# Optimization experiments

Measured on AMD Instinct MI355X. Metric: run time of the kernel, lower is better.

The kernel has to match this reference:

```python
import jax, jax.numpy as jnp
import numpy as np

B, N, E, L = 64, 50000, 1600000, 20
BN_EPS = 1e-5


def setup_inputs() -> dict:
    key = jax.random.key(0)
    ks = jax.random.split(key, 8)
    x = jax.random.normal(ks[0], (B, N), dtype=jnp.float32)
    edge_index = jax.random.randint(ks[1], (2, E), 0, N, dtype=jnp.int32)
    alpha = jax.random.normal(ks[2], (E,), dtype=jnp.float32)
    bias = jax.random.normal(ks[3], (E,), dtype=jnp.float32)
    # LazyLinear(num_labels) on [B, N] features
    W = jax.random.normal(ks[4], (L, N), dtype=jnp.float32) / np.sqrt(N)
    b_lin = jax.random.normal(ks[5], (L,), dtype=jnp.float32) * 0.01
    # LazyBatchNorm1d affine params over N features
    gamma = jnp.ones((N,), dtype=jnp.float32)
    beta = jnp.zeros((N,), dtype=jnp.float32)
    return {"x": x, "edge_index": edge_index, "alpha": alpha, "bias": bias,
            "W": W, "b_lin": b_lin, "gamma": gamma, "beta": beta}


def reference(x, edge_index, alpha, bias, W, b_lin, gamma, beta):
    src, dst = edge_index[0], edge_index[1]
    # gather per-edge source features and apply per-edge affine: [B, E]
    x_e = alpha * x[:, src] + bias
    # scatter-mean into destination nodes: [B, N]
    sums = jnp.zeros((x.shape[0], N), dtype=x.dtype).at[:, dst].add(x_e)
    counts = jnp.zeros((N,), dtype=x.dtype).at[dst].add(1.0)
    x_hat = sums / jnp.maximum(counts, 1.0)
    out = jnp.tanh(x_hat)
    # linear head: [B, L]
    pred = x_hat @ W.T + b_lin
    # BatchNorm1d (training mode: batch stats, biased variance)
    mu = jnp.mean(out, axis=0)
    var = jnp.var(out, axis=0)
    bn = (out - mu) / jnp.sqrt(var + BN_EPS) * gamma + beta
    return (pred, bn)
```

## Files before the change

kernel.cpp:

```cpp
#include <hip/hip_runtime.h>
#include <math.h>

#define NB 64
#define NL 20
#define BN_EPS 1e-5f

#define BIN_W 64
#define NBIN 782
#define NBINP 1024
#define BIN_CAP 2560
#define CHUNK 4096

__device__ __forceinline__ unsigned short f2bf(float f) {
    unsigned u = __float_as_uint(f);
    unsigned r = u + 0x7fff + ((u >> 16) & 1);
    return (unsigned short)(r >> 16);
}
__device__ __forceinline__ float bf2f(unsigned short h) {
    return __uint_as_float(((unsigned)h) << 16);
}

__global__ __launch_bounds__(256) void transpose_kernel(
    const float* __restrict__ x, unsigned short* __restrict__ xTb, int Nn) {
    __shared__ float tile[64][65];
    int n0 = blockIdx.x * 64;
    int ln = threadIdx.x & 63;
    int wv = threadIdx.x >> 6;
    for (int r = wv; r < 64; r += 4) {
        int col = n0 + ln;
        tile[r][ln] = (col < Nn) ? x[r * Nn + col] : 0.f;
    }
    __syncthreads();
    for (int r = wv; r < 64; r += 4) {
        int node = n0 + r;
        if (node < Nn) xTb[(size_t)node * 64 + ln] = f2bf(tile[ln][r]);
    }
}

__global__ __launch_bounds__(1024) void binsort_kernel(
    const int* __restrict__ src, const int* __restrict__ dst,
    const float* __restrict__ alpha, const float* __restrict__ bias,
    int* __restrict__ cursor, uint2* __restrict__ paybins, int E) {
    __shared__ unsigned hist[NBINP];
    __shared__ unsigned scn[NBINP];
    __shared__ unsigned gbase[NBINP];
    __shared__ unsigned wsum[16];
    __shared__ uint2 ord[CHUNK];

    int tid = threadIdx.x;
    int e0 = blockIdx.x * CHUNK;

    hist[tid] = 0;
    __syncthreads();

    uint2 pay[4];
    unsigned rk[4];
    int bn[4];
    #pragma unroll
    for (int k = 0; k < 4; ++k) {
        int e = e0 + k * 1024 + tid;
        bn[k] = -1;
        if (e < E) {
            int d = dst[e];
            int b = d >> 6;
            int dl = d & 63;
            pay[k].x = (unsigned)src[e] | ((unsigned)f2bf(alpha[e]) << 16);
            pay[k].y = (unsigned)f2bf(bias[e]) | ((unsigned)dl << 16) |
                       ((unsigned)b << 22);
            bn[k] = b;
            rk[k] = atomicAdd(&hist[b], 1u);
        }
    }
    __syncthreads();

    unsigned v = hist[tid];
    unsigned incl = v;
    #pragma unroll
    for (int off = 1; off < 64; off <<= 1) {
        unsigned t = __shfl_up(incl, off, 64);
        if ((tid & 63) >= off) incl += t;
    }
    if ((tid & 63) == 63) wsum[tid >> 6] = incl;
    __syncthreads();
    if (tid < 16) {
        unsigned y = wsum[tid];
        unsigned yi = y;
        #pragma unroll
        for (int off = 1; off < 16; off <<= 1) {
            unsigned t = __shfl_up(yi, off, 64);
            if (tid >= off) yi += t;
        }
        wsum[tid] = yi - y;
    }
    __syncthreads();
    unsigned excl = incl - v + wsum[tid >> 6];
    scn[tid] = excl;
    if (v > 0) gbase[tid] = atomicAdd(&cursor[tid], (int)v);
    __syncthreads();

    #pragma unroll
    for (int k = 0; k < 4; ++k)
        if (bn[k] >= 0) ord[scn[bn[k]] + rk[k]] = pay[k];
    __syncthreads();

    int cc = E - e0;
    if (cc > CHUNK) cc = CHUNK;
    for (int p = tid; p < cc; p += 1024) {
        uint2 w = ord[p];
        unsigned b = w.y >> 22;
        unsigned di = gbase[b] + ((unsigned)p - scn[b]);
        if (di < BIN_CAP)
            paybins[(size_t)b * BIN_CAP + di] = w;
    }
}

__global__ __launch_bounds__(512) void pull_fin2_kernel(
    const int* __restrict__ cursor, const uint2* __restrict__ paybins,
    const unsigned short* __restrict__ xTb, const float* __restrict__ W,
    const float* __restrict__ gamma, const float* __restrict__ beta,
    float* __restrict__ pred_part, float* __restrict__ bn, int Nn) {
    __shared__ __align__(16) char smem[33280];
    uint2* ed = (uint2*)smem;
    float (*xh)[65] = (float (*)[65])smem;
    float (*th)[65] = (float (*)[65])(smem + 16640);

    __shared__ float wl[NL][64];
    __shared__ unsigned h2[64], b2[64], c2[64];
    __shared__ float mu_s[64], a_s[64], be_s[64];

    int bin = blockIdx.x;
    int tid = threadIdx.x;
    int ln = tid & 63;
    int w = tid >> 6;
    int n0 = bin * 64;

    int cnt = cursor[bin];
    if (cnt > BIN_CAP) cnt = BIN_CAP;
    const uint2* pb = paybins + (size_t)bin * BIN_CAP;

    for (int i = tid; i < NL * 64; i += 512) {
        int l = i >> 6, j = i & 63;
        wl[l][j] = (n0 + j < Nn) ? W[l * Nn + n0 + j] : 0.f;
    }
    if (tid < 64) { h2[tid] = 0; c2[tid] = 0; }
    __syncthreads();

    uint2 myp[5];
    int nm = 0;
    for (int i = tid; i < cnt; i += 512) {
        uint2 p = pb[i];
        myp[nm++] = p;
        atomicAdd(&h2[(p.y >> 16) & 63], 1u);
    }
    __syncthreads();

    if (tid < 64) {
        unsigned v = h2[tid];
        unsigned incl = v;
        #pragma unroll
        for (int off = 1; off < 64; off <<= 1) {
            unsigned t = __shfl_up(incl, off, 64);
            if (tid >= off) incl += t;
        }
        b2[tid] = incl - v;
    }
    __syncthreads();

    for (int k = 0; k < nm; ++k) {
        unsigned dl = (myp[k].y >> 16) & 63;
        unsigned r = atomicAdd(&c2[dl], 1u);
        ed[b2[dl] + r] = myp[k];
    }
    __syncthreads();

    float xh_reg[8], th_reg[8];
    #pragma unroll
    for (int k = 0; k < 8; ++k) {
        int dl = w * 8 + k;
        int node = n0 + dl;
        int n = (int)h2[dl];
        unsigned bs = b2[dl];
        float a0 = 0.f, a1 = 0.f, a2 = 0.f, a3 = 0.f, bsum = 0.f;
        int j = 0;
        for (; j + 3 < n; j += 4) {
            uint2 e0 = ed[bs + j];
            uint2 e1 = ed[bs + j + 1];
            uint2 e2 = ed[bs + j + 2];
            uint2 e3 = ed[bs + j + 3];
            bsum += __uint_as_float((e0.y & 0xffffu) << 16) +
                    __uint_as_float((e1.y & 0xffffu) << 16) +
                    __uint_as_float((e2.y & 0xffffu) << 16) +
                    __uint_as_float((e3.y & 0xffffu) << 16);
            a0 = fmaf(__uint_as_float(e0.x & 0xffff0000u),
                      bf2f(xTb[(size_t)(e0.x & 0xffffu) * 64 + ln]), a0);
            a1 = fmaf(__uint_as_float(e1.x & 0xffff0000u),
                      bf2f(xTb[(size_t)(e1.x & 0xffffu) * 64 + ln]), a1);
            a2 = fmaf(__uint_as_float(e2.x & 0xffff0000u),
                      bf2f(xTb[(size_t)(e2.x & 0xffffu) * 64 + ln]), a2);
            a3 = fmaf(__uint_as_float(e3.x & 0xffff0000u),
                      bf2f(xTb[(size_t)(e3.x & 0xffffu) * 64 + ln]), a3);
        }
        for (; j < n; ++j) {
            uint2 e0 = ed[bs + j];
            bsum += __uint_as_float((e0.y & 0xffffu) << 16);
            a0 = fmaf(__uint_as_float(e0.x & 0xffff0000u),
                      bf2f(xTb[(size_t)(e0.x & 0xffffu) * 64 + ln]), a0);
        }
        float xhat = 0.f;
        if (node < Nn)
            xhat = ((a0 + a1) + (a2 + a3) + bsum) / fmaxf((float)n, 1.0f);
        xh_reg[k] = xhat;
        float tv = tanhf(xhat);
        th_reg[k] = tv;

        float s = tv, q = tv * tv;
        #pragma unroll
        for (int off = 32; off > 0; off >>= 1) {
            s += __shfl_xor(s, off, 64);
            q += __shfl_xor(q, off, 64);
        }
        if (ln == 0) {
            float mu = s * (1.0f / 64.0f);
            float var = fmaxf(q * (1.0f / 64.0f) - mu * mu, 0.f);
            float inv = rsqrtf(var + BN_EPS);
            float gm = 1.f, bt = 0.f;
            if (node < Nn) { gm = gamma[node]; bt = beta[node]; }
            mu_s[dl] = mu;
            a_s[dl] = inv * gm;
            be_s[dl] = bt;
        }
    }
    __syncthreads();

    #pragma unroll
    for (int k = 0; k < 8; ++k) {
        xh[w * 8 + k][ln] = xh_reg[k];
        th[w * 8 + k][ln] = th_reg[k];
    }
    __syncthreads();

    {
        float acc[3] = {0.f, 0.f, 0.f};
        for (int n = 0; n < 64; ++n) {
            float xv = xh[n][ln];
            #pragma unroll
            for (int k = 0; k < 3; ++k) {
                int l = w + k * 8;
                if (l < NL) acc[k] = fmaf(xv, wl[l][n], acc[k]);
            }
        }
        #pragma unroll
        for (int k = 0; k < 3; ++k) {
            int l = w + k * 8;
            if (l < NL)
                pred_part[(size_t)bin * (NB * NL) + ln * NL + l] = acc[k];
        }
    }

    for (int idx = tid; idx < 64 * 64; idx += 512) {
        int noff = idx & 63, bb = idx >> 6;
        int node = n0 + noff;
        if (node < Nn)
            bn[bb * Nn + node] =
                fmaf(th[noff][bb] - mu_s[noff], a_s[noff], be_s[noff]);
    }
}

__global__ __launch_bounds__(256) void reduce_pred_kernel(
    const float* __restrict__ part, const float* __restrict__ b_lin,
    float* __restrict__ pred, int nblk) {
    int out = blockIdx.x * 4 + (threadIdx.x >> 6);
    if (out >= NB * NL) return;
    int ln = threadIdx.x & 63;
    float s = 0.f;
    for (int i = ln; i < nblk; i += 64)
        s += part[(size_t)i * (NB * NL) + out];
    #pragma unroll
    for (int off = 32; off > 0; off >>= 1)
        s += __shfl_xor(s, off, 64);
    if (ln == 0) pred[out] = b_lin[out % NL] + s;
}

extern "C" void kernel_launch(void* const* d_in, const int* in_sizes, int n_in,
                              void* d_out, int out_size, void* d_ws, size_t ws_size,
                              hipStream_t stream) {
    const float* x     = (const float*)d_in[0];
    const int*   ei    = (const int*)d_in[1];
    const float* alpha = (const float*)d_in[2];
    const float* bias  = (const float*)d_in[3];
    const float* W     = (const float*)d_in[4];
    const float* b_lin = (const float*)d_in[5];
    const float* gamma = (const float*)d_in[6];
    const float* beta  = (const float*)d_in[7];

    const int Nn = in_sizes[0] / NB;
    const int E  = in_sizes[1] / 2;
    const int* src = ei;
    const int* dst = ei + E;

    const int ntile = (Nn + 63) / 64;

    uint2*          paybins = (uint2*)d_ws;
    unsigned short* xTb     = (unsigned short*)(paybins + (size_t)NBIN * BIN_CAP);
    int*            cursor  = (int*)(xTb + (size_t)Nn * 64);
    float*          pred_part = (float*)(cursor + NBIN);

    float* pred = (float*)d_out;
    float* bn   = pred + NB * NL;

    hipMemsetAsync(cursor, 0, NBIN * sizeof(int), stream);

    transpose_kernel<<<ntile, 256, 0, stream>>>(x, xTb, Nn);
    binsort_kernel<<<(E + CHUNK - 1) / CHUNK, 1024, 0, stream>>>(
        src, dst, alpha, bias, cursor, paybins, E);
    pull_fin2_kernel<<<NBIN, 512, 0, stream>>>(cursor, paybins, xTb, W,
                                               gamma, beta, pred_part, bn, Nn);
    reduce_pred_kernel<<<(NB * NL + 3) / 4, 256, 0, stream>>>(
        pred_part, b_lin, pred, NBIN);
}
```

Measured before the change: 212.3 us.

## Halve destination bin width and scatter binned edges directly to global memory

Destination bins shrink from 64 to 32 nodes, which doubles the bin count and halves per-bin capacity. The pull kernel now runs 256-thread blocks over 32 nodes each, with the payload loads unrolled into five fixed registers. The binsort kernel drops the shared-memory local reorder and writes each edge payload straight to its global bin slot, which removes a scan and two barriers but makes the global writes less coalesced. The partial-pred buffer doubles in size, so the final reduction reads twice as much, and the smaller bin capacity raises the risk of dropped edges if a bin overflows.

```diff
diff --git a/kernel.cpp b/kernel.cpp
--- a/kernel.cpp
+++ b/kernel.cpp
@@ -5,10 +5,10 @@
 #define NL 20
 #define BN_EPS 1e-5f
 
-#define BIN_W 64
-#define NBIN 782
-#define NBINP 1024
-#define BIN_CAP 2560
+#define BIN_W 32
+#define NBIN 1563
+#define NBINP 2048
+#define BIN_CAP 1280
 #define CHUNK 4096
 
 __device__ __forceinline__ unsigned short f2bf(float f) {
@@ -42,15 +42,13 @@
     const float* __restrict__ alpha, const float* __restrict__ bias,
     int* __restrict__ cursor, uint2* __restrict__ paybins, int E) {
     __shared__ unsigned hist[NBINP];
-    __shared__ unsigned scn[NBINP];
     __shared__ unsigned gbase[NBINP];
-    __shared__ unsigned wsum[16];
-    __shared__ uint2 ord[CHUNK];
 
     int tid = threadIdx.x;
     int e0 = blockIdx.x * CHUNK;
 
     hist[tid] = 0;
+    hist[tid + 1024] = 0;
     __syncthreads();
 
     uint2 pay[4];
@@ -62,103 +60,85 @@
         bn[k] = -1;
         if (e < E) {
             int d = dst[e];
-            int b = d >> 6;
-            int dl = d & 63;
+            int b = d >> 5;
+            int dl = d & 31;
             pay[k].x = (unsigned)src[e] | ((unsigned)f2bf(alpha[e]) << 16);
             pay[k].y = (unsigned)f2bf(bias[e]) | ((unsigned)dl << 16) |
-                       ((unsigned)b << 22);
+                       ((unsigned)b << 21);
             bn[k] = b;
             rk[k] = atomicAdd(&hist[b], 1u);
         }
     }
     __syncthreads();
 
-    unsigned v = hist[tid];
-    unsigned incl = v;
-    #pragma unroll
-    for (int off = 1; off < 64; off <<= 1) {
-        unsigned t = __shfl_up(incl, off, 64);
-        if ((tid & 63) >= off) incl += t;
-    }
-    if ((tid & 63) == 63) wsum[tid >> 6] = incl;
-    __syncthreads();
-    if (tid < 16) {
-        unsigned y = wsum[tid];
-        unsigned yi = y;
-        #pragma unroll
-        for (int off = 1; off < 16; off <<= 1) {
-            unsigned t = __shfl_up(yi, off, 64);
-            if (tid >= off) yi += t;
-        }
-        wsum[tid] = yi - y;
-    }
-    __syncthreads();
-    unsigned excl = incl - v + wsum[tid >> 6];
-    scn[tid] = excl;
-    if (v > 0) gbase[tid] = atomicAdd(&cursor[tid], (int)v);
-    __syncthreads();
-
-    #pragma unroll
-    for (int k = 0; k < 4; ++k)
-        if (bn[k] >= 0) ord[scn[bn[k]] + rk[k]] = pay[k];
-    __syncthreads();
-
-    int cc = E - e0;
-    if (cc > CHUNK) cc = CHUNK;
-    for (int p = tid; p < cc; p += 1024) {
-        uint2 w = ord[p];
-        unsigned b = w.y >> 22;
-        unsigned di = gbase[b] + ((unsigned)p - scn[b]);
-        if (di < BIN_CAP)
-            paybins[(size_t)b * BIN_CAP + di] = w;
-    }
-}
-
-__global__ __launch_bounds__(512) void pull_fin2_kernel(
+    for (int i = tid; i < NBINP; i += 1024) {
+        unsigned v = hist[i];
+        if (v > 0) gbase[i] = (unsigned)atomicAdd(&cursor[i], (int)v);
+    }
+    __syncthreads();
+
+    #pragma unroll
+    for (int k = 0; k < 4; ++k) {
+        if (bn[k] >= 0) {
+            unsigned di = gbase[bn[k]] + rk[k];
+            if (di < BIN_CAP)
+                paybins[(size_t)bn[k] * BIN_CAP + di] = pay[k];
+        }
+    }
+}
+
+__global__ __launch_bounds__(256) void pull_fin3_kernel(
     const int* __restrict__ cursor, const uint2* __restrict__ paybins,
     const unsigned short* __restrict__ xTb, const float* __restrict__ W,
     const float* __restrict__ gamma, const float* __restrict__ beta,
     float* __restrict__ pred_part, float* __restrict__ bn, int Nn) {
-    __shared__ __align__(16) char smem[33280];
+    __shared__ __align__(16) char smem[16640];
     uint2* ed = (uint2*)smem;
     float (*xh)[65] = (float (*)[65])smem;
-    float (*th)[65] = (float (*)[65])(smem + 16640);
-
-    __shared__ float wl[NL][64];
-    __shared__ unsigned h2[64], b2[64], c2[64];
-    __shared__ float mu_s[64], a_s[64], be_s[64];
+    float (*th)[65] = (float (*)[65])(smem + 8320);
+
+    __shared__ float wl[NL][32];
+    __shared__ unsigned h2[32], b2[32], c2[32];
+    __shared__ float mu_s[32], a_s[32], be_s[32];
 
     int bin = blockIdx.x;
     int tid = threadIdx.x;
     int ln = tid & 63;
     int w = tid >> 6;
-    int n0 = bin * 64;
+    int n0 = bin * 32;
 
     int cnt = cursor[bin];
     if (cnt > BIN_CAP) cnt = BIN_CAP;
     const uint2* pb = paybins + (size_t)bin * BIN_CAP;
 
-    for (int i = tid; i < NL * 64; i += 512) {
-        int l = i >> 6, j = i & 63;
+    for (int i = tid; i < NL * 32; i += 256) {
+        int l = i >> 5, j = i & 31;
         wl[l][j] = (n0 + j < Nn) ? W[l * Nn + n0 + j] : 0.f;
     }
-    if (tid < 64) { h2[tid] = 0; c2[tid] = 0; }
-    __syncthreads();
-
-    uint2 myp[5];
-    int nm = 0;
-    for (int i = tid; i < cnt; i += 512) {
-        uint2 p = pb[i];
-        myp[nm++] = p;
-        atomicAdd(&h2[(p.y >> 16) & 63], 1u);
-    }
-    __syncthreads();
-
-    if (tid < 64) {
+    if (tid < 32) { h2[tid] = 0; c2[tid] = 0; }
+    __syncthreads();
+
+    uint2 pA = {0, 0}, pB = {0, 0}, pC = {0, 0}, pD = {0, 0}, pE = {0, 0};
+    {
+        int i;
+        i = tid;
+        if (i < cnt) { pA = pb[i]; atomicAdd(&h2[(pA.y >> 16) & 31], 1u); }
+        i = tid + 256;
+        if (i < cnt) { pB = pb[i]; atomicAdd(&h2[(pB.y >> 16) & 31], 1u); }
+        i = tid + 512;
+        if (i < cnt) { pC = pb[i]; atomicAdd(&h2[(pC.y >> 16) & 31], 1u); }
+        i = tid + 768;
+        if (i < cnt) { pD = pb[i]; atomicAdd(&h2[(pD.y >> 16) & 31], 1u); }
+        i = tid + 1024;
+        if (i < cnt) { pE = pb[i]; atomicAdd(&h2[(pE.y >> 16) & 31], 1u); }
+    }
+    __syncthreads();
+
+    if (tid < 32) {
         unsigned v = h2[tid];
         unsigned incl = v;
         #pragma unroll
-        for (int off = 1; off < 64; off <<= 1) {
+        for (int off = 1; off < 32; off <<= 1) {
             unsigned t = __shfl_up(incl, off, 64);
             if (tid >= off) incl += t;
         }
@@ -166,10 +146,27 @@
     }
     __syncthreads();
 
-    for (int k = 0; k < nm; ++k) {
-        unsigned dl = (myp[k].y >> 16) & 63;
-        unsigned r = atomicAdd(&c2[dl], 1u);
-        ed[b2[dl] + r] = myp[k];
+    {
+        if (tid < cnt) {
+            unsigned dl = (pA.y >> 16) & 31;
+            ed[b2[dl] + atomicAdd(&c2[dl], 1u)] = pA;
+        }
+        if (tid + 256 < cnt) {
+            unsigned dl = (pB.y >> 16) & 31;
+            ed[b2[dl] + atomicAdd(&c2[dl], 1u)] = pB;
+        }
+        if (tid + 512 < cnt) {
+            unsigned dl = (pC.y >> 16) & 31;
+            ed[b2[dl] + atomicAdd(&c2[dl], 1u)] = pC;
+        }
+        if (tid + 768 < cnt) {
+            unsigned dl = (pD.y >> 16) & 31;
+            ed[b2[dl] + atomicAdd(&c2[dl], 1u)] = pD;
+        }
+        if (tid + 1024 < cnt) {
+            unsigned dl = (pE.y >> 16) & 31;
+            ed[b2[dl] + atomicAdd(&c2[dl], 1u)] = pE;
+        }
     }
     __syncthreads();
 
@@ -240,25 +237,20 @@
     __syncthreads();
 
     {
-        float acc[3] = {0.f, 0.f, 0.f};
-        for (int n = 0; n < 64; ++n) {
+        float acc[5] = {0.f, 0.f, 0.f, 0.f, 0.f};
+        for (int n = 0; n < 32; ++n) {
             float xv = xh[n][ln];
             #pragma unroll
-            for (int k = 0; k < 3; ++k) {
-                int l = w + k * 8;
-                if (l < NL) acc[k] = fmaf(xv, wl[l][n], acc[k]);
-            }
+            for (int k = 0; k < 5; ++k)
+                acc[k] = fmaf(xv, wl[w + k * 4][n], acc[k]);
         }
         #pragma unroll
-        for (int k = 0; k < 3; ++k) {
-            int l = w + k * 8;
-            if (l < NL)
-                pred_part[(size_t)bin * (NB * NL) + ln * NL + l] = acc[k];
-        }
-    }
-
-    for (int idx = tid; idx < 64 * 64; idx += 512) {
-        int noff = idx & 63, bb = idx >> 6;
+        for (int k = 0; k < 5; ++k)
+            pred_part[(size_t)bin * (NB * NL) + ln * NL + (w + k * 4)] = acc[k];
+    }
+
+    for (int idx = tid; idx < 32 * 64; idx += 256) {
+        int noff = idx & 31, bb = idx >> 5;
         int node = n0 + noff;
         if (node < Nn)
             bn[bb * Nn + node] =
@@ -313,7 +305,7 @@
     transpose_kernel<<<ntile, 256, 0, stream>>>(x, xTb, Nn);
     binsort_kernel<<<(E + CHUNK - 1) / CHUNK, 1024, 0, stream>>>(
         src, dst, alpha, bias, cursor, paybins, E);
-    pull_fin2_kernel<<<NBIN, 512, 0, stream>>>(cursor, paybins, xTb, W,
+    pull_fin3_kernel<<<NBIN, 256, 0, stream>>>(cursor, paybins, xTb, W,
                                                gamma, beta, pred_part, bn, Nn);
     reduce_pred_kernel<<<(NB * NL + 3) / 4, 256, 0, stream>>>(
         pred_part, b_lin, pred, NBIN);
```

Result: faster. 194.3 us (-8.5%).
